# Kernel tuning notes

Hardware: AMD Instinct MI355X
Metric: run time of the kernel (lower is better)

## Reference

```python
import jax, jax.numpy as jnp
import numpy as np

DIM = 1024
HEADS = 16
WIN = 7
HEAD_DIM = DIM // HEADS
SCALE = HEAD_DIM ** -0.5
B = 1024
N = WIN * WIN  # 49 tokens per window


def _relative_position_index(window_size: int) -> np.ndarray:
    coords = np.stack(np.meshgrid(np.arange(window_size), np.arange(window_size), indexing='ij'))
    cf = coords.reshape(2, -1)  # [2, N]
    rel = cf[:, :, None] - cf[:, None, :]  # [2, N, N]
    rel = rel.transpose(1, 2, 0)
    rel[:, :, 0] += window_size - 1
    rel[:, :, 1] += window_size - 1
    rel[:, :, 0] *= 2 * window_size - 1
    return rel.sum(-1).astype(np.int32)  # [N, N]


def setup_inputs() -> dict:
    key = jax.random.key(0)
    ks = jax.random.split(key, 12)
    s = 0.02
    inp = {
        'landmark_features': jax.random.normal(ks[0], (B, N, DIM), jnp.float32),
        'image_features': jax.random.normal(ks[1], (B, N, DIM), jnp.float32),
        'Wq': jax.random.normal(ks[2], (DIM, DIM), jnp.float32) * s,
        'bq': jnp.zeros((DIM,), jnp.float32),
        'Wk': jax.random.normal(ks[3], (DIM, DIM), jnp.float32) * s,
        'bk': jnp.zeros((DIM,), jnp.float32),
        'Wv': jax.random.normal(ks[4], (DIM, DIM), jnp.float32) * s,
        'bv': jnp.zeros((DIM,), jnp.float32),
        'Wo': jax.random.normal(ks[5], (DIM, DIM), jnp.float32) * s,
        'bo': jnp.zeros((DIM,), jnp.float32),
        'bias_table': jax.random.normal(ks[6], ((2 * WIN - 1) ** 2, HEADS), jnp.float32) * s,
        'rel_idx': jnp.asarray(_relative_position_index(WIN)),
    }
    return inp


def reference(landmark_features, image_features, Wq, bq, Wk, bk, Wv, bv, Wo, bo, bias_table, rel_idx):
    Bsz, Nk, C = image_features.shape
    # projections (torch Linear: x @ W.T + b), split into heads -> [B, H, N, D]
    def proj(x, W, b):
        y = x @ W.T + b
        return y.reshape(Bsz, -1, HEADS, HEAD_DIM).transpose(0, 2, 1, 3)
    q = proj(landmark_features, Wq, bq)
    k = proj(image_features, Wk, bk)
    v = proj(image_features, Wv, bv)
    attn = jnp.einsum('bhqd,bhkd->bhqk', q, k) * SCALE
    # gathered relative-position bias: [H, N, N]
    bias = bias_table[rel_idx.reshape(-1)].reshape(N, N, HEADS).transpose(2, 0, 1)
    attn = attn + bias[None]
    attn = jax.nn.softmax(attn, axis=-1)
    out = jnp.einsum('bhqk,bhkd->bhqd', attn, v).transpose(0, 2, 1, 3).reshape(Bsz, -1, C)
    return out @ Wo.T + bo
```

## Files before the change

kernel.cpp:

```cpp
#include <hip/hip_runtime.h>

#define DIM 1024
#define HEADS 16
#define HEAD_DIM 64
#define NTOK 49
#define SCALEF 0.125f

typedef __attribute__((ext_vector_type(8))) short bf16x8;
typedef __attribute__((ext_vector_type(4))) float floatx4;

typedef const __attribute__((address_space(1))) void* gptr_t;
typedef __attribute__((address_space(3))) void* sptr_t;

__device__ __forceinline__ void async_load16(const void* g, void* s) {
    __builtin_amdgcn_global_load_lds((gptr_t)g, (sptr_t)s, 16, 0, 0);
}

__device__ __forceinline__ unsigned short f2bf(float f) {
    unsigned int u = __builtin_bit_cast(unsigned int, f);
    u = (u + 0x7fffu + ((u >> 16) & 1u)) >> 16;
    return (unsigned short)u;
}
__device__ __forceinline__ float bf2f(unsigned short s) {
    unsigned int u = ((unsigned int)s) << 16;
    return __builtin_bit_cast(float, u);
}

__global__ void cvt2_kernel(const float* __restrict__ a, const float* __restrict__ b,
                            unsigned short* __restrict__ oa, unsigned short* __restrict__ ob,
                            int n) {
    int i = (blockIdx.x * 256 + threadIdx.x) * 4;
    if (i >= n) return;
    float4 va = *(const float4*)&a[i];
    float4 vb = *(const float4*)&b[i];
    ushort4 ua = make_ushort4(f2bf(va.x), f2bf(va.y), f2bf(va.z), f2bf(va.w));
    ushort4 ub = make_ushort4(f2bf(vb.x), f2bf(vb.y), f2bf(vb.z), f2bf(vb.w));
    *(ushort4*)&oa[i] = ua;
    *(ushort4*)&ob[i] = ub;
}

template <bool OUT_BF16>
__global__ __launch_bounds__(256)
void gemm_bt_kernel(const unsigned short* __restrict__ A,
                    const unsigned short* __restrict__ Bw,
                    const float* __restrict__ bias,
                    void* __restrict__ Cout) {
    constexpr int K = 1024, N = 1024;
    __shared__ unsigned short As[128 * 32];
    __shared__ unsigned short Bs[128 * 32];
    const int tid = threadIdx.x;
    const int lane = tid & 63;
    const int wave = tid >> 6;
    const int wm = (wave >> 1) * 64;
    const int wn = (wave & 1) * 64;
    const int m0 = blockIdx.y * 128;
    const int n0 = blockIdx.x * 128;
    const int lr = lane & 15;
    const int lk = (lane >> 4) * 8;

    floatx4 acc[4][4] = {};

    for (int kt = 0; kt < K / 32; ++kt) {
        const int kbase = kt * 32;
#pragma unroll
        for (int j = 0; j < 2; ++j) {
            int off = tid * 16 + j * 4096;
            int r = off >> 6;
            int ce = (off & 63) >> 1;
            async_load16(A + (size_t)(m0 + r) * K + kbase + ce, (char*)As + off);
            async_load16(Bw + (size_t)(n0 + r) * K + kbase + ce, (char*)Bs + off);
        }
        __syncthreads();
        bf16x8 af[4], bfr[4];
#pragma unroll
        for (int t = 0; t < 4; ++t) {
            af[t]  = *(const bf16x8*)&As[(wm + t * 16 + lr) * 32 + lk];
            bfr[t] = *(const bf16x8*)&Bs[(wn + t * 16 + lr) * 32 + lk];
        }
#pragma unroll
        for (int mt = 0; mt < 4; ++mt)
#pragma unroll
            for (int nt = 0; nt < 4; ++nt)
                acc[mt][nt] = __builtin_amdgcn_mfma_f32_16x16x32_bf16(
                    af[mt], bfr[nt], acc[mt][nt], 0, 0, 0);
        __syncthreads();
    }

#pragma unroll
    for (int mt = 0; mt < 4; ++mt) {
#pragma unroll
        for (int nt = 0; nt < 4; ++nt) {
            int col = n0 + wn + nt * 16 + (lane & 15);
            float bv = bias[col];
#pragma unroll
            for (int r = 0; r < 4; ++r) {
                int row = m0 + wm + mt * 16 + (lane >> 4) * 4 + r;
                float v = acc[mt][nt][r] + bv;
                if (OUT_BF16)
                    ((unsigned short*)Cout)[(size_t)row * N + col] = f2bf(v);
                else
                    ((float*)Cout)[(size_t)row * N + col] = v;
            }
        }
    }
}

#define QKS 68
#define PS 50

__global__ __launch_bounds__(256)
void attn_kernel(const unsigned short* __restrict__ Q,
                 const unsigned short* __restrict__ K,
                 const unsigned short* __restrict__ V,
                 const float* __restrict__ bias_table,
                 const int* __restrict__ rel_idx,
                 unsigned short* __restrict__ ctx) {
    __shared__ float Qs[NTOK * QKS];
    __shared__ float Ks[NTOK * QKS];
    __shared__ float Vs[NTOK * QKS];
    __shared__ float P[NTOK * PS];

    const int tid = threadIdx.x;
    const int bh = blockIdx.x;
    const int h = bh & (HEADS - 1);
    const int b = bh >> 4;
    const size_t rowbase = (size_t)b * NTOK;
    const int colbase = h * HEAD_DIM;

    for (int i = tid; i < NTOK * 16; i += 256) {
        int r = i >> 4;
        int c4 = (i & 15) * 4;
        size_t g = (rowbase + r) * DIM + colbase + c4;
        ushort4 qv = *(const ushort4*)&Q[g];
        ushort4 kv = *(const ushort4*)&K[g];
        ushort4 vv = *(const ushort4*)&V[g];
        float* qd = &Qs[r * QKS + c4];
        float* kd = &Ks[r * QKS + c4];
        float* vd = &Vs[r * QKS + c4];
        qd[0] = bf2f(qv.x); qd[1] = bf2f(qv.y); qd[2] = bf2f(qv.z); qd[3] = bf2f(qv.w);
        kd[0] = bf2f(kv.x); kd[1] = bf2f(kv.y); kd[2] = bf2f(kv.z); kd[3] = bf2f(kv.w);
        vd[0] = bf2f(vv.x); vd[1] = bf2f(vv.y); vd[2] = bf2f(vv.z); vd[3] = bf2f(vv.w);
    }
    __syncthreads();

    for (int item = tid; item < NTOK * 7; item += 256) {
        int q = item / 7;
        int k0 = (item % 7) * 7;
        float s[7] = {0.f, 0.f, 0.f, 0.f, 0.f, 0.f, 0.f};
        const float4* Qr = (const float4*)&Qs[q * QKS];
#pragma unroll 4
        for (int j4 = 0; j4 < 16; ++j4) {
            float4 qv = Qr[j4];
#pragma unroll
            for (int kk = 0; kk < 7; ++kk) {
                float4 kv = *(const float4*)&Ks[(k0 + kk) * QKS + j4 * 4];
                s[kk] += qv.x * kv.x + qv.y * kv.y + qv.z * kv.z + qv.w * kv.w;
            }
        }
#pragma unroll
        for (int kk = 0; kk < 7; ++kk) {
            int k = k0 + kk;
            float bias = bias_table[rel_idx[q * NTOK + k] * HEADS + h];
            P[q * PS + k] = s[kk] * SCALEF + bias;
        }
    }
    __syncthreads();

    if (tid < NTOK) {
        float m = -1e30f;
        for (int k = 0; k < NTOK; ++k) m = fmaxf(m, P[tid * PS + k]);
        float sum = 0.f;
        for (int k = 0; k < NTOK; ++k) {
            float e = __expf(P[tid * PS + k] - m);
            P[tid * PS + k] = e;
            sum += e;
        }
        float inv = 1.f / sum;
        for (int k = 0; k < NTOK; ++k) P[tid * PS + k] *= inv;
    }
    __syncthreads();

    if (tid < 13 * 16) {
        int q0 = (tid >> 4) * 4;
        int d4 = (tid & 15) * 4;
        float ax[4], ay[4], az[4], aw[4];
#pragma unroll
        for (int qi = 0; qi < 4; ++qi) { ax[qi] = ay[qi] = az[qi] = aw[qi] = 0.f; }
        for (int k = 0; k < NTOK; ++k) {
            float4 vv = *(const float4*)&Vs[k * QKS + d4];
#pragma unroll
            for (int qi = 0; qi < 4; ++qi) {
                float p = P[(q0 + qi) * PS + k];
                ax[qi] += p * vv.x; ay[qi] += p * vv.y;
                az[qi] += p * vv.z; aw[qi] += p * vv.w;
            }
        }
#pragma unroll
        for (int qi = 0; qi < 4; ++qi) {
            int q = q0 + qi;
            if (q < NTOK) {
                size_t g = (rowbase + q) * DIM + colbase + d4;
                *(ushort4*)&ctx[g] = make_ushort4(f2bf(ax[qi]), f2bf(ay[qi]),
                                                  f2bf(az[qi]), f2bf(aw[qi]));
            }
        }
    }
}

extern "C" void kernel_launch(void* const* d_in, const int* in_sizes, int n_in,
                              void* d_out, int out_size, void* d_ws, size_t ws_size,
                              hipStream_t stream) {
    const float* landmark = (const float*)d_in[0];
    const float* image    = (const float*)d_in[1];
    const float* Wq = (const float*)d_in[2];
    const float* bq = (const float*)d_in[3];
    const float* Wk = (const float*)d_in[4];
    const float* bk = (const float*)d_in[5];
    const float* Wv = (const float*)d_in[6];
    const float* bv = (const float*)d_in[7];
    const float* Wo = (const float*)d_in[8];
    const float* bo = (const float*)d_in[9];
    const float* bias_table = (const float*)d_in[10];
    const int*   rel_idx    = (const int*)d_in[11];
    float* out = (float*)d_out;

    const size_t FEAT = (size_t)1024 * NTOK * DIM;
    const size_t FB   = FEAT * 2;
    const size_t WB   = (size_t)DIM * DIM * 2;
    char* ws = (char*)d_ws;
    unsigned short* Qb  = (unsigned short*)(ws + 0 * FB);
    unsigned short* Kb  = (unsigned short*)(ws + 1 * FB);
    unsigned short* Vb  = (unsigned short*)(ws + 2 * FB);
    unsigned short* Lb  = (unsigned short*)(ws + 3 * FB);
    unsigned short* Ctx = (unsigned short*)(ws + 3 * FB);
    unsigned short* Ib  = (unsigned short*)(ws + 4 * FB);
    unsigned short* Wqb = (unsigned short*)(ws + 5 * FB + 0 * WB);
    unsigned short* Wkb = (unsigned short*)(ws + 5 * FB + 1 * WB);
    unsigned short* Wvb = (unsigned short*)(ws + 5 * FB + 2 * WB);
    unsigned short* Wob = (unsigned short*)(ws + 5 * FB + 3 * WB);

    cvt2_kernel<<<(int)(FEAT / 4 / 256), 256, 0, stream>>>(landmark, image, Lb, Ib, (int)FEAT);
    cvt2_kernel<<<(int)(DIM * DIM / 4 / 256), 256, 0, stream>>>(Wq, Wk, Wqb, Wkb, DIM * DIM);
    cvt2_kernel<<<(int)(DIM * DIM / 4 / 256), 256, 0, stream>>>(Wv, Wo, Wvb, Wob, DIM * DIM);

    dim3 ggrid(1024 / 128, 50176 / 128);
    gemm_bt_kernel<true><<<ggrid, 256, 0, stream>>>(Lb, Wqb, bq, Qb);
    gemm_bt_kernel<true><<<ggrid, 256, 0, stream>>>(Ib, Wkb, bk, Kb);
    gemm_bt_kernel<true><<<ggrid, 256, 0, stream>>>(Ib, Wvb, bv, Vb);

    attn_kernel<<<1024 * HEADS, 256, 0, stream>>>(Qb, Kb, Vb, bias_table, rel_idx, Ctx);

    gemm_bt_kernel<false><<<ggrid, 256, 0, stream>>>(Ctx, Wob, bo, out);
}
```

Before: 1.447 ms.

## Rewrite windowed attention with bf16 MFMA and register-resident softmax

Replaces the scalar fp32 attention kernel with a one-wave-per-(batch,head) kernel that computes QK^T and PV with bf16 16x16x32 MFMA, pads the 49 tokens to 64, and does softmax in registers with cross-lane shuffles. The relative-position bias is gathered once into a dense padded per-head table (with -inf for padded key columns) by a small precompute kernel, reusing a dead workspace buffer. V is transposed into swizzled LDS and P is written to swizzled LDS to avoid bank conflicts. Padded Q/K rows read adjacent tokens' data and rely on masking, and probabilities are rounded to bf16 before PV.

```diff
diff --git a/kernel.cpp b/kernel.cpp
--- a/kernel.cpp
+++ b/kernel.cpp
@@ -105,103 +105,140 @@
     }
 }
 
-#define QKS 68
-#define PS 50
+__global__ void bias_pre_kernel(const float* __restrict__ bias_table,
+                                const int* __restrict__ rel_idx,
+                                float* __restrict__ bias_dense) {
+    int h = blockIdx.x;
+    for (int i = threadIdx.x; i < 64 * 64; i += 256) {
+        int q = i >> 6, k = i & 63;
+        float v;
+        if (k >= NTOK) v = -1e30f;
+        else if (q >= NTOK) v = 0.f;
+        else v = bias_table[rel_idx[q * NTOK + k] * HEADS + h];
+        bias_dense[h * 4096 + i] = v;
+    }
+}
+
+#define SWZ(row, t) ((t) ^ (((row) & 7) << 3))
 
 __global__ __launch_bounds__(256)
-void attn_kernel(const unsigned short* __restrict__ Q,
-                 const unsigned short* __restrict__ K,
-                 const unsigned short* __restrict__ V,
-                 const float* __restrict__ bias_table,
-                 const int* __restrict__ rel_idx,
-                 unsigned short* __restrict__ ctx) {
-    __shared__ float Qs[NTOK * QKS];
-    __shared__ float Ks[NTOK * QKS];
-    __shared__ float Vs[NTOK * QKS];
-    __shared__ float P[NTOK * PS];
+void attn_mfma_kernel(const unsigned short* __restrict__ Q,
+                      const unsigned short* __restrict__ K,
+                      const unsigned short* __restrict__ V,
+                      const float* __restrict__ bias_dense,
+                      unsigned short* __restrict__ ctx) {
+    __shared__ unsigned short Vt[4][64 * 64];
+    __shared__ unsigned short Pm[4][64 * 64];
 
     const int tid = threadIdx.x;
-    const int bh = blockIdx.x;
-    const int h = bh & (HEADS - 1);
-    const int b = bh >> 4;
-    const size_t rowbase = (size_t)b * NTOK;
-    const int colbase = h * HEAD_DIM;
-
-    for (int i = tid; i < NTOK * 16; i += 256) {
-        int r = i >> 4;
-        int c4 = (i & 15) * 4;
-        size_t g = (rowbase + r) * DIM + colbase + c4;
-        ushort4 qv = *(const ushort4*)&Q[g];
-        ushort4 kv = *(const ushort4*)&K[g];
-        ushort4 vv = *(const ushort4*)&V[g];
-        float* qd = &Qs[r * QKS + c4];
-        float* kd = &Ks[r * QKS + c4];
-        float* vd = &Vs[r * QKS + c4];
-        qd[0] = bf2f(qv.x); qd[1] = bf2f(qv.y); qd[2] = bf2f(qv.z); qd[3] = bf2f(qv.w);
-        kd[0] = bf2f(kv.x); kd[1] = bf2f(kv.y); kd[2] = bf2f(kv.z); kd[3] = bf2f(kv.w);
-        vd[0] = bf2f(vv.x); vd[1] = bf2f(vv.y); vd[2] = bf2f(vv.z); vd[3] = bf2f(vv.w);
-    }
-    __syncthreads();
-
-    for (int item = tid; item < NTOK * 7; item += 256) {
-        int q = item / 7;
-        int k0 = (item % 7) * 7;
-        float s[7] = {0.f, 0.f, 0.f, 0.f, 0.f, 0.f, 0.f};
-        const float4* Qr = (const float4*)&Qs[q * QKS];
-#pragma unroll 4
-        for (int j4 = 0; j4 < 16; ++j4) {
-            float4 qv = Qr[j4];
-#pragma unroll
-            for (int kk = 0; kk < 7; ++kk) {
-                float4 kv = *(const float4*)&Ks[(k0 + kk) * QKS + j4 * 4];
-                s[kk] += qv.x * kv.x + qv.y * kv.y + qv.z * kv.z + qv.w * kv.w;
-            }
-        }
-#pragma unroll
-        for (int kk = 0; kk < 7; ++kk) {
-            int k = k0 + kk;
-            float bias = bias_table[rel_idx[q * NTOK + k] * HEADS + h];
-            P[q * PS + k] = s[kk] * SCALEF + bias;
-        }
-    }
-    __syncthreads();
-
-    if (tid < NTOK) {
-        float m = -1e30f;
-        for (int k = 0; k < NTOK; ++k) m = fmaxf(m, P[tid * PS + k]);
-        float sum = 0.f;
-        for (int k = 0; k < NTOK; ++k) {
-            float e = __expf(P[tid * PS + k] - m);
-            P[tid * PS + k] = e;
-            sum += e;
-        }
-        float inv = 1.f / sum;
-        for (int k = 0; k < NTOK; ++k) P[tid * PS + k] *= inv;
-    }
-    __syncthreads();
-
-    if (tid < 13 * 16) {
-        int q0 = (tid >> 4) * 4;
-        int d4 = (tid & 15) * 4;
-        float ax[4], ay[4], az[4], aw[4];
-#pragma unroll
-        for (int qi = 0; qi < 4; ++qi) { ax[qi] = ay[qi] = az[qi] = aw[qi] = 0.f; }
-        for (int k = 0; k < NTOK; ++k) {
-            float4 vv = *(const float4*)&Vs[k * QKS + d4];
-#pragma unroll
-            for (int qi = 0; qi < 4; ++qi) {
-                float p = P[(q0 + qi) * PS + k];
-                ax[qi] += p * vv.x; ay[qi] += p * vv.y;
-                az[qi] += p * vv.z; aw[qi] += p * vv.w;
-            }
-        }
-#pragma unroll
-        for (int qi = 0; qi < 4; ++qi) {
-            int q = q0 + qi;
-            if (q < NTOK) {
-                size_t g = (rowbase + q) * DIM + colbase + d4;
-                *(ushort4*)&ctx[g] = make_ushort4(f2bf(ax[qi]), f2bf(ay[qi]),
-                                                  f2bf(az[qi]), f2bf(aw[qi]));
+    const int w = tid >> 6;
+    const int lane = tid & 63;
+    const int p = blockIdx.x * 4 + w;
+    const int b = p >> 4;
+    const int h = p & 15;
+    const size_t base = (size_t)(b * NTOK) * DIM + h * HEAD_DIM;
+    unsigned short* vt = Vt[w];
+    unsigned short* pm = Pm[w];
+
+    const int lc = lane & 15;
+    const int lg = lane >> 4;
+
+    for (int i = lane; i < 64 * 16; i += 64) {
+        int tok = i >> 4, d0 = (i & 15) * 4;
+        ushort4 vv = (tok < NTOK) ? *(const ushort4*)&V[base + (size_t)tok * DIM + d0]
+                                  : make_ushort4(0, 0, 0, 0);
+        vt[(d0 + 0) * 64 + SWZ(d0 + 0, tok)] = vv.x;
+        vt[(d0 + 1) * 64 + SWZ(d0 + 1, tok)] = vv.y;
+        vt[(d0 + 2) * 64 + SWZ(d0 + 2, tok)] = vv.z;
+        vt[(d0 + 3) * 64 + SWZ(d0 + 3, tok)] = vv.w;
+    }
+
+    floatx4 acc[4][4] = {};
+#pragma unroll
+    for (int kt = 0; kt < 2; ++kt) {
+        const int d = kt * 32 + lg * 8;
+        bf16x8 af[4], bfr[4];
+#pragma unroll
+        for (int mt = 0; mt < 4; ++mt)
+            af[mt] = *(const bf16x8*)&Q[base + (size_t)(mt * 16 + lc) * DIM + d];
+#pragma unroll
+        for (int nt = 0; nt < 4; ++nt)
+            bfr[nt] = *(const bf16x8*)&K[base + (size_t)(nt * 16 + lc) * DIM + d];
+#pragma unroll
+        for (int mt = 0; mt < 4; ++mt)
+#pragma unroll
+            for (int nt = 0; nt < 4; ++nt)
+                acc[mt][nt] = __builtin_amdgcn_mfma_f32_16x16x32_bf16(
+                    af[mt], bfr[nt], acc[mt][nt], 0, 0, 0);
+    }
+
+    const float* bd = bias_dense + h * 4096;
+#pragma unroll
+    for (int mt = 0; mt < 4; ++mt) {
+#pragma unroll
+        for (int r = 0; r < 4; ++r) {
+            const int row = mt * 16 + lg * 4 + r;
+#pragma unroll
+            for (int nt = 0; nt < 4; ++nt)
+                acc[mt][nt][r] = acc[mt][nt][r] * SCALEF + bd[row * 64 + nt * 16 + lc];
+            float mx = fmaxf(fmaxf(acc[mt][0][r], acc[mt][1][r]),
+                             fmaxf(acc[mt][2][r], acc[mt][3][r]));
+            mx = fmaxf(mx, __shfl_xor(mx, 1));
+            mx = fmaxf(mx, __shfl_xor(mx, 2));
+            mx = fmaxf(mx, __shfl_xor(mx, 4));
+            mx = fmaxf(mx, __shfl_xor(mx, 8));
+            float sm = 0.f;
+#pragma unroll
+            for (int nt = 0; nt < 4; ++nt) {
+                float e = __expf(acc[mt][nt][r] - mx);
+                acc[mt][nt][r] = e;
+                sm += e;
+            }
+            sm += __shfl_xor(sm, 1);
+            sm += __shfl_xor(sm, 2);
+            sm += __shfl_xor(sm, 4);
+            sm += __shfl_xor(sm, 8);
+            const float inv = 1.f / sm;
+#pragma unroll
+            for (int nt = 0; nt < 4; ++nt) {
+                const int col = nt * 16 + lc;
+                pm[row * 64 + SWZ(row, col)] = f2bf(acc[mt][nt][r] * inv);
+            }
+        }
+    }
+
+    floatx4 o[4][4] = {};
+#pragma unroll
+    for (int kt = 0; kt < 2; ++kt) {
+        const int t0 = kt * 32 + lg * 8;
+        bf16x8 af[4], bfr[4];
+#pragma unroll
+        for (int mt = 0; mt < 4; ++mt) {
+            const int q = mt * 16 + lc;
+            af[mt] = *(const bf16x8*)&pm[q * 64 + SWZ(q, t0)];
+        }
+#pragma unroll
+        for (int nt = 0; nt < 4; ++nt) {
+            const int dd = nt * 16 + lc;
+            bfr[nt] = *(const bf16x8*)&vt[dd * 64 + SWZ(dd, t0)];
+        }
+#pragma unroll
+        for (int mt = 0; mt < 4; ++mt)
+#pragma unroll
+            for (int nt = 0; nt < 4; ++nt)
+                o[mt][nt] = __builtin_amdgcn_mfma_f32_16x16x32_bf16(
+                    af[mt], bfr[nt], o[mt][nt], 0, 0, 0);
+    }
+
+#pragma unroll
+    for (int mt = 0; mt < 4; ++mt) {
+#pragma unroll
+        for (int r = 0; r < 4; ++r) {
+            const int row = mt * 16 + lg * 4 + r;
+            if (row < NTOK) {
+#pragma unroll
+                for (int nt = 0; nt < 4; ++nt)
+                    ctx[base + (size_t)row * DIM + nt * 16 + lc] = f2bf(o[mt][nt][r]);
             }
         }
     }
@@ -234,6 +271,7 @@
     unsigned short* Lb  = (unsigned short*)(ws + 3 * FB);
     unsigned short* Ctx = (unsigned short*)(ws + 3 * FB);
     unsigned short* Ib  = (unsigned short*)(ws + 4 * FB);
+    float* bias_dense   = (float*)(ws + 4 * FB);
     unsigned short* Wqb = (unsigned short*)(ws + 5 * FB + 0 * WB);
     unsigned short* Wkb = (unsigned short*)(ws + 5 * FB + 1 * WB);
     unsigned short* Wvb = (unsigned short*)(ws + 5 * FB + 2 * WB);
@@ -248,7 +286,9 @@
     gemm_bt_kernel<true><<<ggrid, 256, 0, stream>>>(Ib, Wkb, bk, Kb);
     gemm_bt_kernel<true><<<ggrid, 256, 0, stream>>>(Ib, Wvb, bv, Vb);
 
-    attn_kernel<<<1024 * HEADS, 256, 0, stream>>>(Qb, Kb, Vb, bias_table, rel_idx, Ctx);
+    bias_pre_kernel<<<HEADS, 256, 0, stream>>>(bias_table, rel_idx, bias_dense);
+
+    attn_mfma_kernel<<<1024 * HEADS / 4, 256, 0, stream>>>(Qb, Kb, Vb, bias_dense, Ctx);
 
     gemm_bt_kernel<false><<<ggrid, 256, 0, stream>>>(Ctx, Wob, bo, out);
 }
```

Measured after the change: 1.319 ms. 8.9% less time.
